# Optimization experiments

Measured on AMD Instinct MI355X. Metric: run time of the kernel, lower is better.

Reference implementation:

```python
import jax, jax.numpy as jnp
import numpy as np

TAU = 250.0   # tau_inv used by all behaviours (norse default / explicit for LLBN)
DT = 0.001
VTH = 30.0
T_STEPS = 10000

# (a, b, c, d) Izhikevich params per cell
LLBN_P = (0.1, -0.075, -55.0, 6.0)      # custom spiking behaviour
EBN_P = (0.02, 0.25, -55.0, 0.05)       # phasic_bursting
IFN_P = (0.02, 0.25, -65.0, 6.0)        # phasic_spiking
TN_P = (0.02, 0.2, -65.0, 6.0)          # tonic_spiking
MN_P = (0.02, 0.25, -65.0, 6.0)         # phasic_spiking


def setup_inputs() -> dict:
    key = jax.random.key(0)
    k1, k2 = jax.random.split(key)
    input_mat = jax.random.uniform(k1, (127, 127), dtype=jnp.float32)
    weights_matrix = jax.random.uniform(k2, (12,), dtype=jnp.float32)
    return {"input_mat": input_mat, "weights_matrix": weights_matrix,
            "nb_repetitions": T_STEPS}


def _izh(v, u, I, p):
    a, b, c, d = p
    v1 = v + TAU * DT * (0.04 * v * v + 5.0 * v + 140.0 - u + I)
    u1 = u + TAU * DT * a * (b * v - u)
    z = (v1 >= VTH).astype(v.dtype)
    return z, jnp.where(z > 0, c, v1), u1 + z * d


def _simulate(input_mat, w, nb_repetitions):
    z_plus = jnp.sum(input_mat * w[0])  # constant across timesteps

    def step(carry, _):
        temp, z2p, v2, u2, v3, u3, v4, u4, z5p, v5, u5, v6, u6 = carry
        # LLBN: recurrent cell, input current = w2*(z_plus*w1 - temp) + w3*z_prev
        z2, v2, u2 = _izh(v2, u2, w[2] * (z_plus * w[1] - temp) + w[3] * z2p, LLBN_P)
        # EBN
        z3, v3, u3 = _izh(v3, u3, z_plus * w[4] + z2 * w[5], EBN_P)
        # IFN (feedback to LLBN via temp, one-step delay)
        z4, v4, u4 = _izh(v4, u4, z3 * w[6], IFN_P)
        temp_n = z4 * w[7]
        # TN: recurrent cell, input current = w9*(z3*w8) + w10*z_prev
        z5, v5, u5 = _izh(v5, u5, w[9] * (z3 * w[8]) + w[10] * z5p, TN_P)
        # MN
        z6, v6, u6 = _izh(v6, u6, z5 * w[11], MN_P)
        new_carry = (temp_n, z2, v2, u2, v3, u3, v4, u4, z5, v5, u5, v6, u6)
        out = (jnp.stack([z2, z3, z4, z5, z6]),  # spikes [5]
               jnp.stack([v2, v3, v4, v5, v6]))  # membrane voltages [5]
        return new_carry, out

    f32 = jnp.float32
    init = (f32(0.0),                      # temp
            f32(0.0), f32(-60.0), f32(4.5),    # LLBN z, v, u (u0 = b*v_rest)
            f32(-64.0), f32(-16.0),            # EBN v, u
            f32(-64.0), f32(-16.0),            # IFN v, u
            f32(0.0), f32(-70.0), f32(-14.0),  # TN z, v, u
            f32(-64.0), f32(-16.0))            # MN v, u
    _, (spikes, volts) = jax.lax.scan(step, init, None, length=nb_repetitions)
    return spikes.T, volts.T  # each [5, T]


def reference(input_mat, weights_matrix, nb_repetitions):
    o_spikes, v = _simulate(input_mat, weights_matrix, nb_repetitions)
    return o_spikes, v
```

## Files before the change

### kernel.cpp

```cpp
#include <hip/hip_runtime.h>

#pragma clang fp contract(off)


__device__ __forceinline__ float sel_mask(float a, float b, unsigned long long m) {
    float r;
    asm("v_cndmask_b32 %0, %1, %2, %3" : "=v"(r) : "v"(a), "v"(b), "s"(m));
    return r;
}

__global__ __launch_bounds__(256) void net_sim(const float* __restrict__ mat,
                                               const float* __restrict__ w,
                                               float* __restrict__ out,
                                               int* __restrict__ ws,
                                               int T) {
    __shared__ double red[256];
    const int tid = threadIdx.x;

    const float w0 = w[0];
    double s = 0.0;
    for (int i = tid; i < 127 * 127; i += 256) {
        float p = mat[i] * w0;
        s += (double)p;
    }
    red[tid] = s;
    __syncthreads();
    #pragma unroll
    for (int off = 128; off > 0; off >>= 1) {
        if (tid < off) red[tid] += red[tid + off];
        __syncthreads();
    }
    if (tid >= 9) return;

    const float z_plus = (float)red[0];

    const float w2 = w[2], w3 = w[3], w5 = w[5], w6 = w[6], w7 = w[7],
                w8 = w[8], w9 = w[9], w10 = w[10], w11 = w[11];
    const float zp_w1 = z_plus * w[1];
    const float zp_w4 = z_plus * w[4];

    const float I2_00 = w2 * (zp_w1 - 0.0f) + w3 * 0.0f;
    const float I2_10 = w2 * (zp_w1 - 0.0f) + w3 * 1.0f;
    const float I2_01 = w2 * (zp_w1 - w7)   + w3 * 0.0f;
    const float I2_11 = w2 * (zp_w1 - w7)   + w3 * 1.0f;
    const float I3_0  = zp_w4 + 0.0f * w5;
    const float I3_1  = zp_w4 + 1.0f * w5;
    const float I4_0  = 0.0f * w6;
    const float I4_1  = 1.0f * w6;
    const float I5_00 = w9 * (0.0f * w8) + w10 * 0.0f;
    const float I5_10 = w9 * (1.0f * w8) + w10 * 0.0f;
    const float I5_01 = w9 * (0.0f * w8) + w10 * 1.0f;
    const float I5_11 = w9 * (1.0f * w8) + w10 * 1.0f;
    const float I6_0  = 0.0f * w11;
    const float I6_1  = 1.0f * w11;

    const int lane = tid;
    const int g = lane == 0 ? 0 : lane <= 2 ? 1 : lane <= 4 ? 2 : lane <= 6 ? 3 : 4;

    const float ka = lane == 0 ? (float)(0.25 * 0.1) : (float)(0.25 * 0.02);
    const float b  = lane == 0 ? -0.075f : (g == 3 ? 0.2f : 0.25f);
    const float c  = g <= 1 ? -55.0f : -65.0f;
    const float d  = g == 1 ? 0.05f : 6.0f;
    float v = g == 0 ? -60.0f : (g == 3 ? -70.0f : -64.0f);
    float u = g == 0 ? 4.5f   : (g == 3 ? -14.0f : -16.0f);

    const float C0a = g == 0 ? I2_00 : g == 1 ? I3_0 : g == 2 ? I4_0
                    : g == 3 ? I5_00 : I6_0;
    const float C0b = g == 0 ? I2_00 : g == 1 ? I3_0 : g == 2 ? I4_0
                    : g == 3 ? I5_01 : I6_0;
    const float C1a = g == 1 ? I3_1 : g == 2 ? I4_1 : g == 3 ? I5_10
                    : g == 4 ? I6_1 : 0.0f;
    const float C1b = g == 1 ? I3_1 : g == 2 ? I4_1 : g == 3 ? I5_11
                    : g == 4 ? I6_1 : 0.0f;

    const bool is_lane0  = (lane == 0);
    const bool spec_var1 = (lane == 2) | (lane == 4) | (lane == 6) | (lane == 8);

    float* __restrict__ psp = out + g * T;
    float* __restrict__ pvv = out + 5 * T + g * T;

    int z2 = 0, z4 = 0, z5 = 0;

    float rav = 0.0f, rau = 0.0f; int raz2 = 0, raz4 = 0, raz5 = 0, ra_t = -1;
    float cav = 0.0f, cau = 0.0f; int caz2 = 0, caz4 = 0, caz5 = 0, ca_t = -1;
    int next_coarse = 8;
    int t_det = -1, Pf = 0;
    int blk5 = 0;

    float zb[8], vb[8];

    int t = 0;
    for (; t + 8 <= T; t += 8) {
        if (blk5 == 0) {
            if (ra_t >= 0) {
                unsigned long long mv =
                    __ballot(__float_as_uint(v) == __float_as_uint(rav));
                unsigned long long mu =
                    __ballot(__float_as_uint(u) == __float_as_uint(rau));
                if (((mv & mu) & 0x1FFull) == 0x1FFull &&
                    z2 == raz2 && z4 == raz4 && z5 == raz5) {
                    t_det = t; Pf = t - ra_t;
                    break;
                }
            }
            if (t) { rav = v; rau = u; raz2 = z2; raz4 = z4; raz5 = z5; ra_t = t; }
        } else if (ca_t >= 0) {
            unsigned long long mv =
                __ballot(__float_as_uint(v) == __float_as_uint(cav));
            unsigned long long mu =
                __ballot(__float_as_uint(u) == __float_as_uint(cau));
            if (((mv & mu) & 0x1FFull) == 0x1FFull &&
                z2 == caz2 && z4 == caz4 && z5 == caz5) {
                t_det = t; Pf = t - ca_t;
                break;
            }
        }
        if (t == next_coarse) {
            cav = v; cau = u; caz2 = z2; caz4 = z4; caz5 = z5; ca_t = t;
            next_coarse <<= 1;
        }
        blk5 = (blk5 == 4) ? 0 : (blk5 + 1);

        #pragma unroll
        for (int j = 0; j < 8; ++j) {
            float fI2 = z4 ? (z2 ? I2_11 : I2_01) : (z2 ? I2_10 : I2_00);
            float V0 = z5 ? C0b : C0a;
            float V1 = z5 ? C1b : C1a;
            V0 = is_lane0 ? fI2 : V0;
            float Ib = spec_var1 ? V1 : V0;

            float t1 = 0.04f * v;
            float t2 = t1 * v;
            float t3 = 5.0f * v;
            float t4 = t2 + t3;
            float t5 = t4 + 140.0f;
            float t6 = t5 - u;
            float bv = b * v;
            float bvu = bv - u;
            float du = ka * bvu;
            float u1 = u + du;

            float t7b = t6 + Ib;
            float v1b = fmaf(0.25f, t7b, v);
            unsigned long long m = __ballot(v1b >= 30.0f);

            int nz2 = (int)(m & 1ull);
            int z3  = (int)((m >> (1 + nz2)) & 1ull);
            int nz4 = (int)((m >> (3 + z3)) & 1ull);
            int nz5 = (int)((m >> (5 + z3)) & 1ull);
            unsigned long long ssel =
                (nz2 ? 0x006ull : 0ull) | (z3 ? 0x078ull : 0ull)
              | (nz5 ? 0x180ull : 0ull);

            float Ia = sel_mask(V0, V1, ssel);
            float t7a = t6 + Ia;
            float v1a = fmaf(0.25f, t7a, v);
            bool fa = (v1a >= 30.0f);
            v = fa ? c : v1a;
            float u1d = u1 + d;
            u = fa ? u1d : u1;

            zb[j] = fa ? 1.0f : 0.0f;
            vb[j] = v;

            z2 = nz2; z4 = nz4; z5 = nz5;
        }
        *(float4*)(psp)     = make_float4(zb[0], zb[1], zb[2], zb[3]);
        *(float4*)(psp + 4) = make_float4(zb[4], zb[5], zb[6], zb[7]);
        *(float4*)(pvv)     = make_float4(vb[0], vb[1], vb[2], vb[3]);
        *(float4*)(pvv + 4) = make_float4(vb[4], vb[5], vb[6], vb[7]);
        psp += 8;
        pvv += 8;
    }
    for (; t < T && t_det < 0; ++t) {
        float fI2 = z4 ? (z2 ? I2_11 : I2_01) : (z2 ? I2_10 : I2_00);
        float V0 = z5 ? C0b : C0a;
        float V1 = z5 ? C1b : C1a;
        V0 = is_lane0 ? fI2 : V0;
        float Ib = spec_var1 ? V1 : V0;
        float t1 = 0.04f * v;
        float t2 = t1 * v;
        float t3 = 5.0f * v;
        float t4 = t2 + t3;
        float t5 = t4 + 140.0f;
        float t6 = t5 - u;
        float bv = b * v;
        float bvu = bv - u;
        float du = ka * bvu;
        float u1 = u + du;
        float t7b = t6 + Ib;
        float v1b = fmaf(0.25f, t7b, v);
        unsigned long long m = __ballot(v1b >= 30.0f);
        int nz2 = (int)(m & 1ull);
        int z3  = (int)((m >> (1 + nz2)) & 1ull);
        int nz4 = (int)((m >> (3 + z3)) & 1ull);
        int nz5 = (int)((m >> (5 + z3)) & 1ull);
        unsigned long long ssel =
            (nz2 ? 0x006ull : 0ull) | (z3 ? 0x078ull : 0ull)
          | (nz5 ? 0x180ull : 0ull);
        float Ia = sel_mask(V0, V1, ssel);
        float t7a = t6 + Ia;
        float v1a = fmaf(0.25f, t7a, v);
        bool fa = (v1a >= 30.0f);
        v = fa ? c : v1a;
        float u1d = u1 + d;
        u = fa ? u1d : u1;
        psp[0] = fa ? 1.0f : 0.0f;
        pvv[0] = v;
        ++psp; ++pvv;
        z2 = nz2; z4 = nz4; z5 = nz5;
    }

    if (lane == 0) {
        ws[0] = (t_det >= 0) ? 1 : 0;
        ws[1] = t_det;
        ws[2] = Pf;
    }
}

__global__ __launch_bounds__(256) void fill_cycle(float* __restrict__ out,
                                                  const int* __restrict__ ws,
                                                  int T) {
    if (ws[0] == 0) return;
    const int t0 = ws[1];
    const int P  = ws[2];
    const int r  = blockIdx.y;
    const float* __restrict__ src = out + (size_t)r * T + (t0 - P);
    float* __restrict__ dst       = out + (size_t)r * T + t0;
    const int n = T - t0;
    for (int i = blockIdx.x * blockDim.x + threadIdx.x; i < n;
         i += gridDim.x * blockDim.x) {
        dst[i] = src[i % P];
    }
}

extern "C" void kernel_launch(void* const* d_in, const int* in_sizes, int n_in,
                              void* d_out, int out_size, void* d_ws, size_t ws_size,
                              hipStream_t stream) {
    const float* mat = (const float*)d_in[0];
    const float* w   = (const float*)d_in[1];
    int T = out_size / 10;
    net_sim<<<1, 256, 0, stream>>>(mat, w, (float*)d_out, (int*)d_ws, T);
    dim3 grid(40, 10, 1);
    fill_cycle<<<grid, 256, 0, stream>>>((float*)d_out, (const int*)d_ws, T);
}
```

Baseline: 293.3 us.

## Compute both input-hypothesis updates per lane and resolve spikes with one ballot chain

Replaces the 9-lane speculative scheme (one lane per cell per hypothesis, plus a second compare pass) with 5 lanes, one per cell. Each lane computes both candidate voltages for the two possible input currents, and two ballots decide the spike chain in order. The final v, u and spike values are then picked with scalar-mask cndmasks instead of a per-lane compare after a second dependent add/fma. This shortens the serial per-step dependency chain, but each step now issues one extra ballot and extra scalar select logic.

```diff
diff --git a/kernel.cpp b/kernel.cpp
--- a/kernel.cpp
+++ b/kernel.cpp
@@ -30,7 +30,7 @@
         if (tid < off) red[tid] += red[tid + off];
         __syncthreads();
     }
-    if (tid >= 9) return;
+    if (tid >= 5) return;
 
     const float z_plus = (float)red[0];
 
@@ -55,29 +55,24 @@
     const float I6_1  = 1.0f * w11;
 
     const int lane = tid;
-    const int g = lane == 0 ? 0 : lane <= 2 ? 1 : lane <= 4 ? 2 : lane <= 6 ? 3 : 4;
-
-    const float ka = lane == 0 ? (float)(0.25 * 0.1) : (float)(0.25 * 0.02);
-    const float b  = lane == 0 ? -0.075f : (g == 3 ? 0.2f : 0.25f);
-    const float c  = g <= 1 ? -55.0f : -65.0f;
-    const float d  = g == 1 ? 0.05f : 6.0f;
-    float v = g == 0 ? -60.0f : (g == 3 ? -70.0f : -64.0f);
-    float u = g == 0 ? 4.5f   : (g == 3 ? -14.0f : -16.0f);
-
-    const float C0a = g == 0 ? I2_00 : g == 1 ? I3_0 : g == 2 ? I4_0
-                    : g == 3 ? I5_00 : I6_0;
-    const float C0b = g == 0 ? I2_00 : g == 1 ? I3_0 : g == 2 ? I4_0
-                    : g == 3 ? I5_01 : I6_0;
-    const float C1a = g == 1 ? I3_1 : g == 2 ? I4_1 : g == 3 ? I5_10
-                    : g == 4 ? I6_1 : 0.0f;
-    const float C1b = g == 1 ? I3_1 : g == 2 ? I4_1 : g == 3 ? I5_11
-                    : g == 4 ? I6_1 : 0.0f;
-
-    const bool is_lane0  = (lane == 0);
-    const bool spec_var1 = (lane == 2) | (lane == 4) | (lane == 6) | (lane == 8);
-
-    float* __restrict__ psp = out + g * T;
-    float* __restrict__ pvv = out + 5 * T + g * T;
+    const bool is_lane0 = (lane == 0);
+
+    const float ka = is_lane0 ? (float)(0.25 * 0.1) : (float)(0.25 * 0.02);
+    const float b  = is_lane0 ? -0.075f : (lane == 3 ? 0.2f : 0.25f);
+    const float c  = lane <= 1 ? -55.0f : -65.0f;
+    const float d  = lane == 1 ? 0.05f : 6.0f;
+    float v = is_lane0 ? -60.0f : (lane == 3 ? -70.0f : -64.0f);
+    float u = is_lane0 ? 4.5f   : (lane == 3 ? -14.0f : -16.0f);
+
+    const float C0a = lane == 1 ? I3_0 : lane == 2 ? I4_0
+                    : lane == 3 ? I5_00 : lane == 4 ? I6_0 : I2_00;
+    const float C0b = lane == 3 ? I5_01 : C0a;
+    const float C1a = lane == 1 ? I3_1 : lane == 2 ? I4_1
+                    : lane == 3 ? I5_10 : lane == 4 ? I6_1 : 0.0f;
+    const float C1b = lane == 3 ? I5_11 : C1a;
+
+    float* __restrict__ psp = out + lane * T;
+    float* __restrict__ pvv = out + 5 * T + lane * T;
 
     int z2 = 0, z4 = 0, z5 = 0;
 
@@ -97,7 +92,7 @@
                     __ballot(__float_as_uint(v) == __float_as_uint(rav));
                 unsigned long long mu =
                     __ballot(__float_as_uint(u) == __float_as_uint(rau));
-                if (((mv & mu) & 0x1FFull) == 0x1FFull &&
+                if (((mv & mu) & 0x1Full) == 0x1Full &&
                     z2 == raz2 && z4 == raz4 && z5 == raz5) {
                     t_det = t; Pf = t - ra_t;
                     break;
@@ -109,7 +104,7 @@
                 __ballot(__float_as_uint(v) == __float_as_uint(cav));
             unsigned long long mu =
                 __ballot(__float_as_uint(u) == __float_as_uint(cau));
-            if (((mv & mu) & 0x1FFull) == 0x1FFull &&
+            if (((mv & mu) & 0x1Full) == 0x1Full &&
                 z2 == caz2 && z4 == caz4 && z5 == caz5) {
                 t_det = t; Pf = t - ca_t;
                 break;
@@ -127,7 +122,6 @@
             float V0 = z5 ? C0b : C0a;
             float V1 = z5 ? C1b : C1a;
             V0 = is_lane0 ? fI2 : V0;
-            float Ib = spec_var1 ? V1 : V0;
 
             float t1 = 0.04f * v;
             float t2 = t1 * v;
@@ -139,28 +133,36 @@
             float bvu = bv - u;
             float du = ka * bvu;
             float u1 = u + du;
-
-            float t7b = t6 + Ib;
-            float v1b = fmaf(0.25f, t7b, v);
-            unsigned long long m = __ballot(v1b >= 30.0f);
-
-            int nz2 = (int)(m & 1ull);
-            int z3  = (int)((m >> (1 + nz2)) & 1ull);
-            int nz4 = (int)((m >> (3 + z3)) & 1ull);
-            int nz5 = (int)((m >> (5 + z3)) & 1ull);
+            float u1d = u1 + d;
+
+            float t7_0 = t6 + V0;
+            float t7_1 = t6 + V1;
+            float v1_0 = fmaf(0.25f, t7_0, v);
+            float v1_1 = fmaf(0.25f, t7_1, v);
+            unsigned long long m0 = __ballot(v1_0 >= 30.0f);
+            unsigned long long m1 = __ballot(v1_1 >= 30.0f);
+
+            unsigned a0 = (unsigned)m0, a1 = (unsigned)m1;
+            int nz2 = (int)(a0 & 1u);
+            unsigned selE = nz2 ? a1 : a0;
+            int z3  = (int)((selE >> 1) & 1u);
+            unsigned sel3 = z3 ? a1 : a0;
+            int nz4 = (int)((sel3 >> 2) & 1u);
+            int nz5 = (int)((sel3 >> 3) & 1u);
+            unsigned selM = nz5 ? a1 : a0;
+            int nz6 = (int)((selM >> 4) & 1u);
             unsigned long long ssel =
-                (nz2 ? 0x006ull : 0ull) | (z3 ? 0x078ull : 0ull)
-              | (nz5 ? 0x180ull : 0ull);
-
-            float Ia = sel_mask(V0, V1, ssel);
-            float t7a = t6 + Ia;
-            float v1a = fmaf(0.25f, t7a, v);
-            bool fa = (v1a >= 30.0f);
-            v = fa ? c : v1a;
-            float u1d = u1 + d;
-            u = fa ? u1d : u1;
-
-            zb[j] = fa ? 1.0f : 0.0f;
+                (nz2 ? 0x02ull : 0ull) | (z3 ? 0x0Cull : 0ull)
+              | (nz5 ? 0x10ull : 0ull);
+            unsigned long long fm =
+                (nz2 ? 0x01ull : 0ull) | (z3 ? 0x02ull : 0ull)
+              | (nz4 ? 0x04ull : 0ull) | (nz5 ? 0x08ull : 0ull)
+              | (nz6 ? 0x10ull : 0ull);
+
+            float v1s = sel_mask(v1_0, v1_1, ssel);
+            v = sel_mask(v1s, c, fm);
+            u = sel_mask(u1, u1d, fm);
+            zb[j] = sel_mask(0.0f, 1.0f, fm);
             vb[j] = v;
 
             z2 = nz2; z4 = nz4; z5 = nz5;
@@ -177,7 +179,6 @@
         float V0 = z5 ? C0b : C0a;
         float V1 = z5 ? C1b : C1a;
         V0 = is_lane0 ? fI2 : V0;
-        float Ib = spec_var1 ? V1 : V0;
         float t1 = 0.04f * v;
         float t2 = t1 * v;
         float t3 = 5.0f * v;
@@ -188,24 +189,33 @@
         float bvu = bv - u;
         float du = ka * bvu;
         float u1 = u + du;
-        float t7b = t6 + Ib;
-        float v1b = fmaf(0.25f, t7b, v);
-        unsigned long long m = __ballot(v1b >= 30.0f);
-        int nz2 = (int)(m & 1ull);
-        int z3  = (int)((m >> (1 + nz2)) & 1ull);
-        int nz4 = (int)((m >> (3 + z3)) & 1ull);
-        int nz5 = (int)((m >> (5 + z3)) & 1ull);
+        float u1d = u1 + d;
+        float t7_0 = t6 + V0;
+        float t7_1 = t6 + V1;
+        float v1_0 = fmaf(0.25f, t7_0, v);
+        float v1_1 = fmaf(0.25f, t7_1, v);
+        unsigned long long m0 = __ballot(v1_0 >= 30.0f);
+        unsigned long long m1 = __ballot(v1_1 >= 30.0f);
+        unsigned a0 = (unsigned)m0, a1 = (unsigned)m1;
+        int nz2 = (int)(a0 & 1u);
+        unsigned selE = nz2 ? a1 : a0;
+        int z3  = (int)((selE >> 1) & 1u);
+        unsigned sel3 = z3 ? a1 : a0;
+        int nz4 = (int)((sel3 >> 2) & 1u);
+        int nz5 = (int)((sel3 >> 3) & 1u);
+        unsigned selM = nz5 ? a1 : a0;
+        int nz6 = (int)((selM >> 4) & 1u);
         unsigned long long ssel =
-            (nz2 ? 0x006ull : 0ull) | (z3 ? 0x078ull : 0ull)
-          | (nz5 ? 0x180ull : 0ull);
-        float Ia = sel_mask(V0, V1, ssel);
-        float t7a = t6 + Ia;
-        float v1a = fmaf(0.25f, t7a, v);
-        bool fa = (v1a >= 30.0f);
-        v = fa ? c : v1a;
-        float u1d = u1 + d;
-        u = fa ? u1d : u1;
-        psp[0] = fa ? 1.0f : 0.0f;
+            (nz2 ? 0x02ull : 0ull) | (z3 ? 0x0Cull : 0ull)
+          | (nz5 ? 0x10ull : 0ull);
+        unsigned long long fm =
+            (nz2 ? 0x01ull : 0ull) | (z3 ? 0x02ull : 0ull)
+          | (nz4 ? 0x04ull : 0ull) | (nz5 ? 0x08ull : 0ull)
+          | (nz6 ? 0x10ull : 0ull);
+        float v1s = sel_mask(v1_0, v1_1, ssel);
+        v = sel_mask(v1s, c, fm);
+        u = sel_mask(u1, u1d, fm);
+        psp[0] = sel_mask(0.0f, 1.0f, fm);
         pvv[0] = v;
         ++psp; ++pvv;
         z2 = nz2; z4 = nz4; z5 = nz5;
```

Measured after the change: 303.5 us. +3.5%, slower.

## Speculate two timesteps per ballot using extra lanes for second-step branches

Applied to the files above, without the earlier changes.

Extends the speculative per-lane evaluation from 9 to 23 lanes so each wave ballot resolves the spike pattern for two consecutive timesteps instead of one. Extra lanes compute the second step under every possible first-step spike combination, and the actual cascade is then decoded from the mask. This halves the number of serial ballot round trips on the latency-bound recurrence, at the cost of more arithmetic per step, a longer decode chain and more live registers.

```diff
diff --git a/kernel.cpp b/kernel.cpp
--- a/kernel.cpp
+++ b/kernel.cpp
@@ -30,7 +30,7 @@
         if (tid < off) red[tid] += red[tid + off];
         __syncthreads();
     }
-    if (tid >= 9) return;
+    if (tid >= 23) return;
 
     const float z_plus = (float)red[0];
 
@@ -55,32 +55,49 @@
     const float I6_1  = 1.0f * w11;
 
     const int lane = tid;
-    const int g = lane == 0 ? 0 : lane <= 2 ? 1 : lane <= 4 ? 2 : lane <= 6 ? 3 : 4;
-
-    const float ka = lane == 0 ? (float)(0.25 * 0.1) : (float)(0.25 * 0.02);
-    const float b  = lane == 0 ? -0.075f : (g == 3 ? 0.2f : 0.25f);
+    const int g = (lane == 0 || lane == 9 || lane == 10) ? 0
+                : (lane == 1 || lane == 2 || (lane >= 11 && lane <= 14)) ? 1
+                : (lane == 3 || lane == 4 || (lane >= 15 && lane <= 18)) ? 2
+                : (lane == 5 || lane == 6 || (lane >= 19 && lane <= 22)) ? 3 : 4;
+    const bool isL = (g == 0);
+    const bool s2  = (lane >= 9);
+    const int  bbit = s2 ? (1 - (lane & 1)) : 0;
+
+    const float ka = isL ? (float)(0.25 * 0.1) : (float)(0.25 * 0.02);
+    const float b  = isL ? -0.075f : (g == 3 ? 0.2f : 0.25f);
     const float c  = g <= 1 ? -55.0f : -65.0f;
     const float d  = g == 1 ? 0.05f : 6.0f;
-    float v = g == 0 ? -60.0f : (g == 3 ? -70.0f : -64.0f);
-    float u = g == 0 ? 4.5f   : (g == 3 ? -14.0f : -16.0f);
+    float v = isL ? -60.0f : (g == 3 ? -70.0f : -64.0f);
+    float u = isL ? 4.5f   : (g == 3 ? -14.0f : -16.0f);
 
     const float C0a = g == 0 ? I2_00 : g == 1 ? I3_0 : g == 2 ? I4_0
                     : g == 3 ? I5_00 : I6_0;
-    const float C0b = g == 0 ? I2_00 : g == 1 ? I3_0 : g == 2 ? I4_0
-                    : g == 3 ? I5_01 : I6_0;
+    const float C0b = g == 3 ? I5_01 : C0a;
     const float C1a = g == 1 ? I3_1 : g == 2 ? I4_1 : g == 3 ? I5_10
                     : g == 4 ? I6_1 : 0.0f;
-    const float C1b = g == 1 ? I3_1 : g == 2 ? I4_1 : g == 3 ? I5_11
-                    : g == 4 ? I6_1 : 0.0f;
-
-    const bool is_lane0  = (lane == 0);
-    const bool spec_var1 = (lane == 2) | (lane == 4) | (lane == 6) | (lane == 8);
+    const float C1b = g == 3 ? I5_11 : C1a;
+
+    const bool sv1 = (lane == 2) | (lane == 4) | (lane == 6) | (lane == 8)
+                   | (lane == 13) | (lane == 14) | (lane == 17) | (lane == 18)
+                   | (lane == 21) | (lane == 22);
+
+    const float JT0 = !s2 ? 0.0f
+                    : g == 0 ? (bbit ? I2_01 : I2_00)
+                    : g == 1 ? (bbit ? I3_1 : I3_0)
+                    : g == 2 ? (bbit ? I4_1 : I4_0)
+                    :          (bbit ? I5_10 : I5_00);
+    const float JT1 = !s2 ? 0.0f
+                    : g == 0 ? (bbit ? I2_11 : I2_10)
+                    : g == 1 ? (bbit ? I3_1 : I3_0)
+                    : g == 2 ? (bbit ? I4_1 : I4_0)
+                    :          (bbit ? I5_11 : I5_01);
 
     float* __restrict__ psp = out + g * T;
     float* __restrict__ pvv = out + 5 * T + g * T;
 
-    int z2 = 0, z4 = 0, z5 = 0;
-
+    int z2c = 0, z4c = 0, z5c = 0;
+
+    const unsigned long long MASKL = 0x7FFFFFull;
     float rav = 0.0f, rau = 0.0f; int raz2 = 0, raz4 = 0, raz5 = 0, ra_t = -1;
     float cav = 0.0f, cau = 0.0f; int caz2 = 0, caz4 = 0, caz5 = 0, ca_t = -1;
     int next_coarse = 8;
@@ -97,73 +114,101 @@
                     __ballot(__float_as_uint(v) == __float_as_uint(rav));
                 unsigned long long mu =
                     __ballot(__float_as_uint(u) == __float_as_uint(rau));
-                if (((mv & mu) & 0x1FFull) == 0x1FFull &&
-                    z2 == raz2 && z4 == raz4 && z5 == raz5) {
+                if (((mv & mu) & MASKL) == MASKL &&
+                    z2c == raz2 && z4c == raz4 && z5c == raz5) {
                     t_det = t; Pf = t - ra_t;
                     break;
                 }
             }
-            if (t) { rav = v; rau = u; raz2 = z2; raz4 = z4; raz5 = z5; ra_t = t; }
+            if (t) { rav = v; rau = u; raz2 = z2c; raz4 = z4c; raz5 = z5c; ra_t = t; }
         } else if (ca_t >= 0) {
             unsigned long long mv =
                 __ballot(__float_as_uint(v) == __float_as_uint(cav));
             unsigned long long mu =
                 __ballot(__float_as_uint(u) == __float_as_uint(cau));
-            if (((mv & mu) & 0x1FFull) == 0x1FFull &&
-                z2 == caz2 && z4 == caz4 && z5 == caz5) {
+            if (((mv & mu) & MASKL) == MASKL &&
+                z2c == caz2 && z4c == caz4 && z5c == caz5) {
                 t_det = t; Pf = t - ca_t;
                 break;
             }
         }
         if (t == next_coarse) {
-            cav = v; cau = u; caz2 = z2; caz4 = z4; caz5 = z5; ca_t = t;
+            cav = v; cau = u; caz2 = z2c; caz4 = z4c; caz5 = z5c; ca_t = t;
             next_coarse <<= 1;
         }
         blk5 = (blk5 == 4) ? 0 : (blk5 + 1);
 
         #pragma unroll
-        for (int j = 0; j < 8; ++j) {
-            float fI2 = z4 ? (z2 ? I2_11 : I2_01) : (z2 ? I2_10 : I2_00);
-            float V0 = z5 ? C0b : C0a;
-            float V1 = z5 ? C1b : C1a;
-            V0 = is_lane0 ? fI2 : V0;
-            float Ib = spec_var1 ? V1 : V0;
-
-            float t1 = 0.04f * v;
-            float t2 = t1 * v;
-            float t3 = 5.0f * v;
-            float t4 = t2 + t3;
-            float t5 = t4 + 140.0f;
-            float t6 = t5 - u;
-            float bv = b * v;
-            float bvu = bv - u;
-            float du = ka * bvu;
-            float u1 = u + du;
-
-            float t7b = t6 + Ib;
-            float v1b = fmaf(0.25f, t7b, v);
-            unsigned long long m = __ballot(v1b >= 30.0f);
-
-            int nz2 = (int)(m & 1ull);
-            int z3  = (int)((m >> (1 + nz2)) & 1ull);
-            int nz4 = (int)((m >> (3 + z3)) & 1ull);
-            int nz5 = (int)((m >> (5 + z3)) & 1ull);
-            unsigned long long ssel =
-                (nz2 ? 0x006ull : 0ull) | (z3 ? 0x078ull : 0ull)
-              | (nz5 ? 0x180ull : 0ull);
-
-            float Ia = sel_mask(V0, V1, ssel);
+        for (int j = 0; j < 4; ++j) {
+            float fI2 = z4c ? (z2c ? I2_11 : I2_01) : (z2c ? I2_10 : I2_00);
+            float V0s = z5c ? C0b : C0a;
+            float V1s = z5c ? C1b : C1a;
+            V0s = isL ? fI2 : V0s;
+            float Ib1 = sv1 ? V1s : V0s;
+
+            float t1 = 0.04f * v;  float t2 = t1 * v;  float t3 = 5.0f * v;
+            float t4 = t2 + t3;    float t5 = t4 + 140.0f; float t6 = t5 - u;
+            float bv = b * v;      float bvu = bv - u;  float du = ka * bvu;
+            float u1 = u + du;     float u1d = u1 + d;
+            float t7 = t6 + Ib1;
+            float v1b = fmaf(0.25f, t7, v);
+            bool f1 = (v1b >= 30.0f);
+
+            float vs = f1 ? c : v1b;
+            float us = f1 ? u1d : u1;
+            float J  = f1 ? JT1 : JT0;
+            float q1 = 0.04f * vs; float q2 = q1 * vs; float q3 = 5.0f * vs;
+            float q4 = q2 + q3;    float q5 = q4 + 140.0f; float q6 = q5 - us;
+            float q7 = q6 + J;
+            float v2b = fmaf(0.25f, q7, vs);
+            bool f2 = (v2b >= 30.0f);
+
+            bool bbsel = s2 ? f2 : f1;
+            unsigned m = (unsigned)__ballot(bbsel);
+
+            int z2t = (int)(m & 1u);
+            int z3t = (int)((m >> (1 + z2t)) & 1u);
+            int z4t = (int)((m >> (3 + z3t)) & 1u);
+            int z5t = (int)((m >> (5 + z3t)) & 1u);
+            int z2n = (int)((m >> (9 + z4t)) & 1u);
+            int z3n = (int)((m >> (11 + 2 * z2t + z2n)) & 1u);
+            int s34 = 2 * z3t + z3n;
+            int z4n = (int)((m >> (15 + s34)) & 1u);
+            int z5n = (int)((m >> (19 + s34)) & 1u);
+            unsigned long long ssel1 =
+                  (z2t ? 0x7806ull : 0ull) | (z3t ? 0x7F8078ull : 0ull)
+                | (z5t ? 0x180ull : 0ull);
+            unsigned long long ssel2 =
+                  (z2n ? 0x7806ull : 0ull) | (z3n ? 0x7F8078ull : 0ull)
+                | (z5n ? 0x180ull : 0ull);
+
+            float Ia = sel_mask(V0s, V1s, ssel1);
             float t7a = t6 + Ia;
             float v1a = fmaf(0.25f, t7a, v);
             bool fa = (v1a >= 30.0f);
-            v = fa ? c : v1a;
-            float u1d = u1 + d;
-            u = fa ? u1d : u1;
-
-            zb[j] = fa ? 1.0f : 0.0f;
-            vb[j] = v;
-
-            z2 = nz2; z4 = nz4; z5 = nz5;
+            float vA = fa ? c : v1a;
+            float uA = fa ? u1d : u1;
+            zb[2 * j] = fa ? 1.0f : 0.0f;
+            vb[2 * j] = vA;
+
+            float fI2p = z4t ? (z2t ? I2_11 : I2_01) : (z2t ? I2_10 : I2_00);
+            float V0n = z5t ? C0b : C0a;
+            float V1n = z5t ? C1b : C1a;
+            V0n = isL ? fI2p : V0n;
+            float Ia2 = sel_mask(V0n, V1n, ssel2);
+            float r1 = 0.04f * vA; float r2 = r1 * vA; float r3 = 5.0f * vA;
+            float r4 = r2 + r3;    float r5 = r4 + 140.0f; float r6 = r5 - uA;
+            float bvA = b * vA;    float bvuA = bvA - uA; float duA = ka * bvuA;
+            float uB = uA + duA;   float uBd = uB + d;
+            float r7 = r6 + Ia2;
+            float v2a = fmaf(0.25f, r7, vA);
+            bool fa2 = (v2a >= 30.0f);
+            v = fa2 ? c : v2a;
+            u = fa2 ? uBd : uB;
+            zb[2 * j + 1] = fa2 ? 1.0f : 0.0f;
+            vb[2 * j + 1] = v;
+
+            z2c = z2n; z4c = z4n; z5c = z5n;
         }
         *(float4*)(psp)     = make_float4(zb[0], zb[1], zb[2], zb[3]);
         *(float4*)(psp + 4) = make_float4(zb[4], zb[5], zb[6], zb[7]);
@@ -173,42 +218,36 @@
         pvv += 8;
     }
     for (; t < T && t_det < 0; ++t) {
-        float fI2 = z4 ? (z2 ? I2_11 : I2_01) : (z2 ? I2_10 : I2_00);
-        float V0 = z5 ? C0b : C0a;
-        float V1 = z5 ? C1b : C1a;
-        V0 = is_lane0 ? fI2 : V0;
-        float Ib = spec_var1 ? V1 : V0;
-        float t1 = 0.04f * v;
-        float t2 = t1 * v;
-        float t3 = 5.0f * v;
-        float t4 = t2 + t3;
-        float t5 = t4 + 140.0f;
-        float t6 = t5 - u;
-        float bv = b * v;
-        float bvu = bv - u;
-        float du = ka * bvu;
-        float u1 = u + du;
-        float t7b = t6 + Ib;
-        float v1b = fmaf(0.25f, t7b, v);
-        unsigned long long m = __ballot(v1b >= 30.0f);
-        int nz2 = (int)(m & 1ull);
-        int z3  = (int)((m >> (1 + nz2)) & 1ull);
-        int nz4 = (int)((m >> (3 + z3)) & 1ull);
-        int nz5 = (int)((m >> (5 + z3)) & 1ull);
-        unsigned long long ssel =
-            (nz2 ? 0x006ull : 0ull) | (z3 ? 0x078ull : 0ull)
-          | (nz5 ? 0x180ull : 0ull);
-        float Ia = sel_mask(V0, V1, ssel);
+        float fI2 = z4c ? (z2c ? I2_11 : I2_01) : (z2c ? I2_10 : I2_00);
+        float V0s = z5c ? C0b : C0a;
+        float V1s = z5c ? C1b : C1a;
+        V0s = isL ? fI2 : V0s;
+        float Ib1 = sv1 ? V1s : V0s;
+        float t1 = 0.04f * v;  float t2 = t1 * v;  float t3 = 5.0f * v;
+        float t4 = t2 + t3;    float t5 = t4 + 140.0f; float t6 = t5 - u;
+        float bv = b * v;      float bvu = bv - u;  float du = ka * bvu;
+        float u1 = u + du;     float u1d = u1 + d;
+        float t7 = t6 + Ib1;
+        float v1b = fmaf(0.25f, t7, v);
+        bool f1 = (v1b >= 30.0f);
+        unsigned m = (unsigned)__ballot(f1);
+        int z2t = (int)(m & 1u);
+        int z3t = (int)((m >> (1 + z2t)) & 1u);
+        int z4t = (int)((m >> (3 + z3t)) & 1u);
+        int z5t = (int)((m >> (5 + z3t)) & 1u);
+        unsigned long long ssel1 =
+              (z2t ? 0x7806ull : 0ull) | (z3t ? 0x7F8078ull : 0ull)
+            | (z5t ? 0x180ull : 0ull);
+        float Ia = sel_mask(V0s, V1s, ssel1);
         float t7a = t6 + Ia;
         float v1a = fmaf(0.25f, t7a, v);
         bool fa = (v1a >= 30.0f);
         v = fa ? c : v1a;
-        float u1d = u1 + d;
         u = fa ? u1d : u1;
         psp[0] = fa ? 1.0f : 0.0f;
         pvv[0] = v;
         ++psp; ++pvv;
-        z2 = nz2; z4 = nz4; z5 = nz5;
+        z2c = z2t; z4c = z4t; z5c = z5t;
     }
 
     if (lane == 0) {
```

New measurement: 315.3 us. 7.5% more time.

## Replace lane-parallel speculative cell update with serial per-thread five-cell chain

Applied to the files above, without the earlier changes.

Before, each of the five neurons ran on its own lane (nine lanes with speculation) and ballots resolved the dependencies between cells. Now a single thread runs all five cells serially each step, with the selects done as ordinary scalar branches. This removes the cross-lane ballot and mask work from the critical path and replaces it with a longer dependent arithmetic chain. The unroll drops from 8 to 4 steps, cycle detection compares all state registers directly, and only thread 0 writes outputs.

```diff
diff --git a/kernel.cpp b/kernel.cpp
--- a/kernel.cpp
+++ b/kernel.cpp
@@ -2,12 +2,6 @@
 
 #pragma clang fp contract(off)
 
-
-__device__ __forceinline__ float sel_mask(float a, float b, unsigned long long m) {
-    float r;
-    asm("v_cndmask_b32 %0, %1, %2, %3" : "=v"(r) : "v"(a), "v"(b), "s"(m));
-    return r;
-}
 
 __global__ __launch_bounds__(256) void net_sim(const float* __restrict__ mat,
                                                const float* __restrict__ w,
@@ -30,7 +24,7 @@
         if (tid < off) red[tid] += red[tid + off];
         __syncthreads();
     }
-    if (tid >= 9) return;
+    if (tid >= 32) return;
 
     const float z_plus = (float)red[0];
 
@@ -54,164 +48,199 @@
     const float I6_0  = 0.0f * w11;
     const float I6_1  = 1.0f * w11;
 
-    const int lane = tid;
-    const int g = lane == 0 ? 0 : lane <= 2 ? 1 : lane <= 4 ? 2 : lane <= 6 ? 3 : 4;
-
-    const float ka = lane == 0 ? (float)(0.25 * 0.1) : (float)(0.25 * 0.02);
-    const float b  = lane == 0 ? -0.075f : (g == 3 ? 0.2f : 0.25f);
-    const float c  = g <= 1 ? -55.0f : -65.0f;
-    const float d  = g == 1 ? 0.05f : 6.0f;
-    float v = g == 0 ? -60.0f : (g == 3 ? -70.0f : -64.0f);
-    float u = g == 0 ? 4.5f   : (g == 3 ? -14.0f : -16.0f);
-
-    const float C0a = g == 0 ? I2_00 : g == 1 ? I3_0 : g == 2 ? I4_0
-                    : g == 3 ? I5_00 : I6_0;
-    const float C0b = g == 0 ? I2_00 : g == 1 ? I3_0 : g == 2 ? I4_0
-                    : g == 3 ? I5_01 : I6_0;
-    const float C1a = g == 1 ? I3_1 : g == 2 ? I4_1 : g == 3 ? I5_10
-                    : g == 4 ? I6_1 : 0.0f;
-    const float C1b = g == 1 ? I3_1 : g == 2 ? I4_1 : g == 3 ? I5_11
-                    : g == 4 ? I6_1 : 0.0f;
-
-    const bool is_lane0  = (lane == 0);
-    const bool spec_var1 = (lane == 2) | (lane == 4) | (lane == 6) | (lane == 8);
-
-    float* __restrict__ psp = out + g * T;
-    float* __restrict__ pvv = out + 5 * T + g * T;
-
-    int z2 = 0, z4 = 0, z5 = 0;
-
-    float rav = 0.0f, rau = 0.0f; int raz2 = 0, raz4 = 0, raz5 = 0, ra_t = -1;
-    float cav = 0.0f, cau = 0.0f; int caz2 = 0, caz4 = 0, caz5 = 0, ca_t = -1;
+    const float kaL = (float)(0.25 * 0.1);
+    const float kaO = (float)(0.25 * 0.02);
+
+    float v2 = -60.0f, u2 = 4.5f;
+    float v3 = -64.0f, u3 = -16.0f;
+    float v4 = -64.0f, u4 = -16.0f;
+    float v5 = -70.0f, u5 = -14.0f;
+    float v6 = -64.0f, u6 = -16.0f;
+    int z2p = 0, z4p = 0, z5p = 0;
+
+    float* p0 = out;           float* q0 = out + 5 * T;
+    float* p1 = out + T;       float* q1 = out + 6 * T;
+    float* p2 = out + 2 * T;   float* q2 = out + 7 * T;
+    float* p3 = out + 3 * T;   float* q3 = out + 8 * T;
+    float* p4 = out + 4 * T;   float* q4 = out + 9 * T;
+
+    float rv2=0,ru2=0,rv3=0,ru3=0,rv4=0,ru4=0,rv5=0,ru5=0,rv6=0,ru6=0;
+    int rz2=0, rz4=0, rz5=0, ra_t=-1;
+    float cv2=0,cu2=0,cv3=0,cu3=0,cv4=0,cu4=0,cv5=0,cu5=0,cv6=0,cu6=0;
+    int cz2=0, cz4=0, cz5=0, ca_t=-1;
     int next_coarse = 8;
     int t_det = -1, Pf = 0;
-    int blk5 = 0;
-
-    float zb[8], vb[8];
+    int blk10 = 0;
+
+    float zbL[4], zbE[4], zbI[4], zbT[4], zbM[4];
+    float vbL[4], vbE[4], vbI[4], vbT[4], vbM[4];
 
     int t = 0;
-    for (; t + 8 <= T; t += 8) {
-        if (blk5 == 0) {
+    for (; t + 4 <= T; t += 4) {
+        if (blk10 == 0) {
             if (ra_t >= 0) {
-                unsigned long long mv =
-                    __ballot(__float_as_uint(v) == __float_as_uint(rav));
-                unsigned long long mu =
-                    __ballot(__float_as_uint(u) == __float_as_uint(rau));
-                if (((mv & mu) & 0x1FFull) == 0x1FFull &&
-                    z2 == raz2 && z4 == raz4 && z5 == raz5) {
-                    t_det = t; Pf = t - ra_t;
-                    break;
-                }
+                bool eq =
+                    (__float_as_uint(v2) == __float_as_uint(rv2)) &&
+                    (__float_as_uint(u2) == __float_as_uint(ru2)) &&
+                    (__float_as_uint(v3) == __float_as_uint(rv3)) &&
+                    (__float_as_uint(u3) == __float_as_uint(ru3)) &&
+                    (__float_as_uint(v4) == __float_as_uint(rv4)) &&
+                    (__float_as_uint(u4) == __float_as_uint(ru4)) &&
+                    (__float_as_uint(v5) == __float_as_uint(rv5)) &&
+                    (__float_as_uint(u5) == __float_as_uint(ru5)) &&
+                    (__float_as_uint(v6) == __float_as_uint(rv6)) &&
+                    (__float_as_uint(u6) == __float_as_uint(ru6)) &&
+                    (z2p == rz2) && (z4p == rz4) && (z5p == rz5);
+                if (eq) { t_det = t; Pf = t - ra_t; break; }
             }
-            if (t) { rav = v; rau = u; raz2 = z2; raz4 = z4; raz5 = z5; ra_t = t; }
+            if (t) {
+                rv2=v2; ru2=u2; rv3=v3; ru3=u3; rv4=v4; ru4=u4;
+                rv5=v5; ru5=u5; rv6=v6; ru6=u6;
+                rz2=z2p; rz4=z4p; rz5=z5p; ra_t=t;
+            }
         } else if (ca_t >= 0) {
-            unsigned long long mv =
-                __ballot(__float_as_uint(v) == __float_as_uint(cav));
-            unsigned long long mu =
-                __ballot(__float_as_uint(u) == __float_as_uint(cau));
-            if (((mv & mu) & 0x1FFull) == 0x1FFull &&
-                z2 == caz2 && z4 == caz4 && z5 == caz5) {
-                t_det = t; Pf = t - ca_t;
-                break;
-            }
+            bool eq =
+                (__float_as_uint(v2) == __float_as_uint(cv2)) &&
+                (__float_as_uint(u2) == __float_as_uint(cu2)) &&
+                (__float_as_uint(v3) == __float_as_uint(cv3)) &&
+                (__float_as_uint(u3) == __float_as_uint(cu3)) &&
+                (__float_as_uint(v4) == __float_as_uint(cv4)) &&
+                (__float_as_uint(u4) == __float_as_uint(cu4)) &&
+                (__float_as_uint(v5) == __float_as_uint(cv5)) &&
+                (__float_as_uint(u5) == __float_as_uint(cu5)) &&
+                (__float_as_uint(v6) == __float_as_uint(cv6)) &&
+                (__float_as_uint(u6) == __float_as_uint(cu6)) &&
+                (z2p == cz2) && (z4p == cz4) && (z5p == cz5);
+            if (eq) { t_det = t; Pf = t - ca_t; break; }
         }
         if (t == next_coarse) {
-            cav = v; cau = u; caz2 = z2; caz4 = z4; caz5 = z5; ca_t = t;
+            cv2=v2; cu2=u2; cv3=v3; cu3=u3; cv4=v4; cu4=u4;
+            cv5=v5; cu5=u5; cv6=v6; cu6=u6;
+            cz2=z2p; cz4=z4p; cz5=z5p; ca_t=t;
             next_coarse <<= 1;
         }
-        blk5 = (blk5 == 4) ? 0 : (blk5 + 1);
+        blk10 = (blk10 == 9) ? 0 : (blk10 + 1);
 
         #pragma unroll
-        for (int j = 0; j < 8; ++j) {
-            float fI2 = z4 ? (z2 ? I2_11 : I2_01) : (z2 ? I2_10 : I2_00);
-            float V0 = z5 ? C0b : C0a;
-            float V1 = z5 ? C1b : C1a;
-            V0 = is_lane0 ? fI2 : V0;
-            float Ib = spec_var1 ? V1 : V0;
-
-            float t1 = 0.04f * v;
-            float t2 = t1 * v;
-            float t3 = 5.0f * v;
-            float t4 = t2 + t3;
-            float t5 = t4 + 140.0f;
-            float t6 = t5 - u;
-            float bv = b * v;
-            float bvu = bv - u;
-            float du = ka * bvu;
-            float u1 = u + du;
-
-            float t7b = t6 + Ib;
-            float v1b = fmaf(0.25f, t7b, v);
-            unsigned long long m = __ballot(v1b >= 30.0f);
-
-            int nz2 = (int)(m & 1ull);
-            int z3  = (int)((m >> (1 + nz2)) & 1ull);
-            int nz4 = (int)((m >> (3 + z3)) & 1ull);
-            int nz5 = (int)((m >> (5 + z3)) & 1ull);
-            unsigned long long ssel =
-                (nz2 ? 0x006ull : 0ull) | (z3 ? 0x078ull : 0ull)
-              | (nz5 ? 0x180ull : 0ull);
-
-            float Ia = sel_mask(V0, V1, ssel);
-            float t7a = t6 + Ia;
-            float v1a = fmaf(0.25f, t7a, v);
-            bool fa = (v1a >= 30.0f);
-            v = fa ? c : v1a;
-            float u1d = u1 + d;
-            u = fa ? u1d : u1;
-
-            zb[j] = fa ? 1.0f : 0.0f;
-            vb[j] = v;
-
-            z2 = nz2; z4 = nz4; z5 = nz5;
-        }
-        *(float4*)(psp)     = make_float4(zb[0], zb[1], zb[2], zb[3]);
-        *(float4*)(psp + 4) = make_float4(zb[4], zb[5], zb[6], zb[7]);
-        *(float4*)(pvv)     = make_float4(vb[0], vb[1], vb[2], vb[3]);
-        *(float4*)(pvv + 4) = make_float4(vb[4], vb[5], vb[6], vb[7]);
-        psp += 8;
-        pvv += 8;
+        for (int j = 0; j < 4; ++j) {
+            float I2 = z4p ? (z2p ? I2_11 : I2_01) : (z2p ? I2_10 : I2_00);
+            float La1 = 0.04f * v2; float La2 = La1 * v2; float La3 = 5.0f * v2;
+            float La4 = La2 + La3;  float La5 = La4 + 140.0f; float La6 = La5 - u2;
+            float Lbv = -0.075f * v2; float Lbu = Lbv - u2; float Ldu = kaL * Lbu;
+            float Lu1 = u2 + Ldu;   float Lud = Lu1 + 6.0f;
+            float Lt7 = La6 + I2;   float Lv1 = fmaf(0.25f, Lt7, v2);
+            bool Z2 = (Lv1 >= 30.0f);
+            v2 = Z2 ? -55.0f : Lv1;  u2 = Z2 ? Lud : Lu1;
+
+            float I3 = Z2 ? I3_1 : I3_0;
+            float Ea1 = 0.04f * v3; float Ea2 = Ea1 * v3; float Ea3 = 5.0f * v3;
+            float Ea4 = Ea2 + Ea3;  float Ea5 = Ea4 + 140.0f; float Ea6 = Ea5 - u3;
+            float Ebv = 0.25f * v3; float Ebu = Ebv - u3; float Edu = kaO * Ebu;
+            float Eu1 = u3 + Edu;   float Eud = Eu1 + 0.05f;
+            float Et7 = Ea6 + I3;   float Ev1 = fmaf(0.25f, Et7, v3);
+            bool Z3 = (Ev1 >= 30.0f);
+            v3 = Z3 ? -55.0f : Ev1;  u3 = Z3 ? Eud : Eu1;
+
+            float I4 = Z3 ? I4_1 : I4_0;
+            float Fa1 = 0.04f * v4; float Fa2 = Fa1 * v4; float Fa3 = 5.0f * v4;
+            float Fa4 = Fa2 + Fa3;  float Fa5 = Fa4 + 140.0f; float Fa6 = Fa5 - u4;
+            float Fbv = 0.25f * v4; float Fbu = Fbv - u4; float Fdu = kaO * Fbu;
+            float Fu1 = u4 + Fdu;   float Fud = Fu1 + 6.0f;
+            float Ft7 = Fa6 + I4;   float Fv1 = fmaf(0.25f, Ft7, v4);
+            bool Z4 = (Fv1 >= 30.0f);
+            v4 = Z4 ? -65.0f : Fv1;  u4 = Z4 ? Fud : Fu1;
+
+            float I5 = z5p ? (Z3 ? I5_11 : I5_01) : (Z3 ? I5_10 : I5_00);
+            float Ta1 = 0.04f * v5; float Ta2 = Ta1 * v5; float Ta3 = 5.0f * v5;
+            float Ta4 = Ta2 + Ta3;  float Ta5 = Ta4 + 140.0f; float Ta6 = Ta5 - u5;
+            float Tbv = 0.2f * v5;  float Tbu = Tbv - u5; float Tdu = kaO * Tbu;
+            float Tu1 = u5 + Tdu;   float Tud = Tu1 + 6.0f;
+            float Tt7 = Ta6 + I5;   float Tv1 = fmaf(0.25f, Tt7, v5);
+            bool Z5 = (Tv1 >= 30.0f);
+            v5 = Z5 ? -65.0f : Tv1;  u5 = Z5 ? Tud : Tu1;
+
+            float I6 = Z5 ? I6_1 : I6_0;
+            float Ma1 = 0.04f * v6; float Ma2 = Ma1 * v6; float Ma3 = 5.0f * v6;
+            float Ma4 = Ma2 + Ma3;  float Ma5 = Ma4 + 140.0f; float Ma6 = Ma5 - u6;
+            float Mbv = 0.25f * v6; float Mbu = Mbv - u6; float Mdu = kaO * Mbu;
+            float Mu1 = u6 + Mdu;   float Mud = Mu1 + 6.0f;
+            float Mt7 = Ma6 + I6;   float Mv1 = fmaf(0.25f, Mt7, v6);
+            bool Z6 = (Mv1 >= 30.0f);
+            v6 = Z6 ? -65.0f : Mv1;  u6 = Z6 ? Mud : Mu1;
+
+            zbL[j] = Z2 ? 1.0f : 0.0f;  vbL[j] = v2;
+            zbE[j] = Z3 ? 1.0f : 0.0f;  vbE[j] = v3;
+            zbI[j] = Z4 ? 1.0f : 0.0f;  vbI[j] = v4;
+            zbT[j] = Z5 ? 1.0f : 0.0f;  vbT[j] = v5;
+            zbM[j] = Z6 ? 1.0f : 0.0f;  vbM[j] = v6;
+
+            z2p = Z2; z4p = Z4; z5p = Z5;
+        }
+        if (tid == 0) {
+            *(float4*)(p0 + t) = make_float4(zbL[0], zbL[1], zbL[2], zbL[3]);
+            *(float4*)(p1 + t) = make_float4(zbE[0], zbE[1], zbE[2], zbE[3]);
+            *(float4*)(p2 + t) = make_float4(zbI[0], zbI[1], zbI[2], zbI[3]);
+            *(float4*)(p3 + t) = make_float4(zbT[0], zbT[1], zbT[2], zbT[3]);
+            *(float4*)(p4 + t) = make_float4(zbM[0], zbM[1], zbM[2], zbM[3]);
+            *(float4*)(q0 + t) = make_float4(vbL[0], vbL[1], vbL[2], vbL[3]);
+            *(float4*)(q1 + t) = make_float4(vbE[0], vbE[1], vbE[2], vbE[3]);
+            *(float4*)(q2 + t) = make_float4(vbI[0], vbI[1], vbI[2], vbI[3]);
+            *(float4*)(q3 + t) = make_float4(vbT[0], vbT[1], vbT[2], vbT[3]);
+            *(float4*)(q4 + t) = make_float4(vbM[0], vbM[1], vbM[2], vbM[3]);
+        }
     }
     for (; t < T && t_det < 0; ++t) {
-        float fI2 = z4 ? (z2 ? I2_11 : I2_01) : (z2 ? I2_10 : I2_00);
-        float V0 = z5 ? C0b : C0a;
-        float V1 = z5 ? C1b : C1a;
-        V0 = is_lane0 ? fI2 : V0;
-        float Ib = spec_var1 ? V1 : V0;
-        float t1 = 0.04f * v;
-        float t2 = t1 * v;
-        float t3 = 5.0f * v;
-        float t4 = t2 + t3;
-        float t5 = t4 + 140.0f;
-        float t6 = t5 - u;
-        float bv = b * v;
-        float bvu = bv - u;
-        float du = ka * bvu;
-        float u1 = u + du;
-        float t7b = t6 + Ib;
-        float v1b = fmaf(0.25f, t7b, v);
-        unsigned long long m = __ballot(v1b >= 30.0f);
-        int nz2 = (int)(m & 1ull);
-        int z3  = (int)((m >> (1 + nz2)) & 1ull);
-        int nz4 = (int)((m >> (3 + z3)) & 1ull);
-        int nz5 = (int)((m >> (5 + z3)) & 1ull);
-        unsigned long long ssel =
-            (nz2 ? 0x006ull : 0ull) | (z3 ? 0x078ull : 0ull)
-          | (nz5 ? 0x180ull : 0ull);
-        float Ia = sel_mask(V0, V1, ssel);
-        float t7a = t6 + Ia;
-        float v1a = fmaf(0.25f, t7a, v);
-        bool fa = (v1a >= 30.0f);
-        v = fa ? c : v1a;
-        float u1d = u1 + d;
-        u = fa ? u1d : u1;
-        psp[0] = fa ? 1.0f : 0.0f;
-        pvv[0] = v;
-        ++psp; ++pvv;
-        z2 = nz2; z4 = nz4; z5 = nz5;
-    }
-
-    if (lane == 0) {
+        float I2 = z4p ? (z2p ? I2_11 : I2_01) : (z2p ? I2_10 : I2_00);
+        float La1 = 0.04f * v2; float La2 = La1 * v2; float La3 = 5.0f * v2;
+        float La4 = La2 + La3;  float La5 = La4 + 140.0f; float La6 = La5 - u2;
+        float Lbv = -0.075f * v2; float Lbu = Lbv - u2; float Ldu = kaL * Lbu;
+        float Lu1 = u2 + Ldu;   float Lud = Lu1 + 6.0f;
+        float Lt7 = La6 + I2;   float Lv1 = fmaf(0.25f, Lt7, v2);
+        bool Z2 = (Lv1 >= 30.0f);
+        v2 = Z2 ? -55.0f : Lv1;  u2 = Z2 ? Lud : Lu1;
+        float I3 = Z2 ? I3_1 : I3_0;
+        float Ea1 = 0.04f * v3; float Ea2 = Ea1 * v3; float Ea3 = 5.0f * v3;
+        float Ea4 = Ea2 + Ea3;  float Ea5 = Ea4 + 140.0f; float Ea6 = Ea5 - u3;
+        float Ebv = 0.25f * v3; float Ebu = Ebv - u3; float Edu = kaO * Ebu;
+        float Eu1 = u3 + Edu;   float Eud = Eu1 + 0.05f;
+        float Et7 = Ea6 + I3;   float Ev1 = fmaf(0.25f, Et7, v3);
+        bool Z3 = (Ev1 >= 30.0f);
+        v3 = Z3 ? -55.0f : Ev1;  u3 = Z3 ? Eud : Eu1;
+        float I4 = Z3 ? I4_1 : I4_0;
+        float Fa1 = 0.04f * v4; float Fa2 = Fa1 * v4; float Fa3 = 5.0f * v4;
+        float Fa4 = Fa2 + Fa3;  float Fa5 = Fa4 + 140.0f; float Fa6 = Fa5 - u4;
+        float Fbv = 0.25f * v4; float Fbu = Fbv - u4; float Fdu = kaO * Fbu;
+        float Fu1 = u4 + Fdu;   float Fud = Fu1 + 6.0f;
+        float Ft7 = Fa6 + I4;   float Fv1 = fmaf(0.25f, Ft7, v4);
+        bool Z4 = (Fv1 >= 30.0f);
+        v4 = Z4 ? -65.0f : Fv1;  u4 = Z4 ? Fud : Fu1;
+        float I5 = z5p ? (Z3 ? I5_11 : I5_01) : (Z3 ? I5_10 : I5_00);
+        float Ta1 = 0.04f * v5; float Ta2 = Ta1 * v5; float Ta3 = 5.0f * v5;
+        float Ta4 = Ta2 + Ta3;  float Ta5 = Ta4 + 140.0f; float Ta6 = Ta5 - u5;
+        float Tbv = 0.2f * v5;  float Tbu = Tbv - u5; float Tdu = kaO * Tbu;
+        float Tu1 = u5 + Tdu;   float Tud = Tu1 + 6.0f;
+        float Tt7 = Ta6 + I5;   float Tv1 = fmaf(0.25f, Tt7, v5);
+        bool Z5 = (Tv1 >= 30.0f);
+        v5 = Z5 ? -65.0f : Tv1;  u5 = Z5 ? Tud : Tu1;
+        float I6 = Z5 ? I6_1 : I6_0;
+        float Ma1 = 0.04f * v6; float Ma2 = Ma1 * v6; float Ma3 = 5.0f * v6;
+        float Ma4 = Ma2 + Ma3;  float Ma5 = Ma4 + 140.0f; float Ma6 = Ma5 - u6;
+        float Mbv = 0.25f * v6; float Mbu = Mbv - u6; float Mdu = kaO * Mbu;
+        float Mu1 = u6 + Mdu;   float Mud = Mu1 + 6.0f;
+        float Mt7 = Ma6 + I6;   float Mv1 = fmaf(0.25f, Mt7, v6);
+        bool Z6 = (Mv1 >= 30.0f);
+        v6 = Z6 ? -65.0f : Mv1;  u6 = Z6 ? Mud : Mu1;
+        if (tid == 0) {
+            p0[t] = Z2 ? 1.0f : 0.0f;  q0[t] = v2;
+            p1[t] = Z3 ? 1.0f : 0.0f;  q1[t] = v3;
+            p2[t] = Z4 ? 1.0f : 0.0f;  q2[t] = v4;
+            p3[t] = Z5 ? 1.0f : 0.0f;  q3[t] = v5;
+            p4[t] = Z6 ? 1.0f : 0.0f;  q4[t] = v6;
+        }
+        z2p = Z2; z4p = Z4; z5p = Z5;
+    }
+
+    if (tid == 0) {
         ws[0] = (t_det >= 0) ? 1 : 0;
         ws[1] = t_det;
         ws[2] = Pf;
```

Result: slower. 502.8 us (+71.4%).
